# Optimization experiments

Hardware: AMD Instinct MI355X
Metric: run time of the kernel (lower is better)

The kernel has to match this reference:

```python
import jax, jax.numpy as jnp
import numpy as np

# Scalars from init_kwargs (qat_training=False inference path)
IN_ZP = 0
OUT_ZP = 0
IN_SCALE = 0.02
OUT_SCALE = 0.05
STRIDE = (1, 1)
PAD = (1, 1)      # (ph, pw); module pads (pw, pw, ph, ph) via F.pad
DIL = (1, 1)
GROUPS = 1
QMIN, QMAX = -128, 127  # get_quantized_range(8)


def setup_inputs() -> dict:
    key = jax.random.key(0)
    k1, k2, k3, k4 = jax.random.split(key, 4)
    x = jax.random.randint(k1, (32, 128, 56, 56), -128, 128, dtype=jnp.int32).astype(jnp.int8)
    weight = jax.random.randint(k2, (256, 128, 3, 3), -128, 128, dtype=jnp.int32).astype(jnp.int8)
    bias = jax.random.randint(k3, (256,), -1000, 1000, dtype=jnp.int32)
    weight_scale = jax.random.uniform(k4, (256,), minval=1e-3, maxval=1e-2, dtype=jnp.float32)
    return {"x": x, "weight": weight, "bias": bias, "weight_scale": weight_scale}


def reference(x, weight, bias, weight_scale):
    # Pad spatial dims with the input zero point (matches F.pad(..., value=input_zero_point))
    xp = jnp.pad(x.astype(jnp.int32),
                 ((0, 0), (0, 0), (PAD[0], PAD[0]), (PAD[1], PAD[1])),
                 constant_values=IN_ZP)
    # Exact int32-accumulate convolution (torch CPU path)
    acc = jax.lax.conv_general_dilated(
        xp, weight.astype(jnp.int32),
        window_strides=STRIDE, padding='VALID', rhs_dilation=DIL,
        dimension_numbers=('NCHW', 'OIHW', 'NCHW'),
        feature_group_count=GROUPS, preferred_element_type=jnp.int32)
    acc = acc + bias[None, :, None, None]
    # Per-output-channel requantization
    scale = (IN_SCALE * weight_scale / OUT_SCALE)[None, :, None, None]
    out = acc.astype(jnp.float32) * scale + OUT_ZP
    out = jnp.clip(jnp.round(out), QMIN, QMAX).astype(jnp.int8)
    return out
```

## Files before the change

### kernel.cpp

```cpp
#include <hip/hip_runtime.h>
#include <hip/hip_bf16.h>
#include <stdint.h>


#define NB   32
#define CIN  128
#define HO   56
#define WO   56
#define KOUT 256
#define HP   58
#define ROWB (HP * CIN)

typedef int v4i  __attribute__((ext_vector_type(4)));
typedef int v16i __attribute__((ext_vector_type(16)));

static __device__ __forceinline__ void gload_lds16(const int8_t* g, int8_t* l) {
  __builtin_amdgcn_global_load_lds(
      (const __attribute__((address_space(1))) void*)g,
      (__attribute__((address_space(3))) void*)l, 16, 0, 0);
}

__global__ __launch_bounds__(256) void pack_x_kernel(const int* __restrict__ x,
                                                     int8_t* __restrict__ xp) {
  __shared__ int t32[128][57];
  const int tid = threadIdx.x;
  const int r = blockIdx.x;
  const int n = blockIdx.y;
  const bool interior = (r >= 1) && (r <= HO);

  if (interior) {
    const int h = r - 1;
    const int* xrow = x + ((size_t)(n * CIN) * HO + h) * WO;
    #pragma unroll
    for (int it = 0; it < 7; ++it) {
      const int j = it * 256 + tid;
      const int c = j / 14;
      const int w4 = j - c * 14;
      const int4 v = *reinterpret_cast<const int4*>(xrow + c * 3136 + w4 * 4);
      t32[c][w4 * 4 + 0] = v.x;
      t32[c][w4 * 4 + 1] = v.y;
      t32[c][w4 * 4 + 2] = v.z;
      t32[c][w4 * 4 + 3] = v.w;
    }
  }
  __syncthreads();
  #pragma unroll
  for (int it = 0; it < 8; ++it) {
    const int i = it * 256 + tid;
    if (i < HP * 32) {
      const int w = i >> 5;
      const int c4 = i & 31;
      int vv = 0;
      if (interior && w >= 1 && w <= WO) {
        const int b0 = t32[c4 * 4 + 0][w - 1] & 0xff;
        const int b1 = t32[c4 * 4 + 1][w - 1] & 0xff;
        const int b2 = t32[c4 * 4 + 2][w - 1] & 0xff;
        const int b3 = t32[c4 * 4 + 3][w - 1];
        vv = b0 | (b1 << 8) | (b2 << 16) | (b3 << 24);
      }
      *reinterpret_cast<int*>(xp + ((size_t)(n * HP + r) * HP + w) * CIN + c4 * 4) = vv;
    }
  }
}

__global__ __launch_bounds__(256) void pack_w_kernel(const int* __restrict__ wgt,
                                                     int8_t* __restrict__ wq) {
  const int wid = blockIdx.x * 256 + threadIdx.x;
  const int wi = wid & 3;
  const int ci = wid >> 2;
  const int kt = ci / 4608;
  const int r  = ci - kt * 4608;
  const int tap = r >> 9;
  const int r2  = r & 511;
  const int cc  = r2 >> 6;
  const int ch  = r2 & 63;
  const int k_global = kt * 64 + ch;
  const int cin0 = cc * 16 + wi * 4;
  const int base = (k_global * CIN + cin0) * 9 + tap;
  const int v0 = wgt[base];
  const int v1 = wgt[base + 9];
  const int v2 = wgt[base + 18];
  const int v3 = wgt[base + 27];
  reinterpret_cast<int*>(wq)[wid] =
      (v0 & 0xff) | ((v1 & 0xff) << 8) | ((v2 & 0xff) << 16) | (v3 << 24);
}

__global__ __launch_bounds__(512, 2) void conv_kernel(const int8_t* __restrict__ xp,
                                                      const int8_t* __restrict__ wq,
                                                      const int* __restrict__ bias,
                                                      const float* __restrict__ wscale,
                                                      int* __restrict__ out) {
  __shared__ __align__(16) int8_t lw[9 * 8 * 64 * 16];
  __shared__ __align__(16) int8_t lx[10 * HP * 8 * 16];
  __shared__ int   bsh[64];
  __shared__ float ssh[64];

  const int tid = threadIdx.x;
  const int kt = blockIdx.x;
  const int h0 = blockIdx.y * 8;
  const int n_img = blockIdx.z;

  const int lane = tid & 63;
  const int wr = tid >> 6;
  const int p0 = lane & 31;
  const int half = lane >> 5;

  const int8_t* xg = xp + ((size_t)(n_img * HP) + h0) * ROWB;
  const int8_t* wqt = wq + (size_t)kt * 73728;

  #pragma unroll
  for (int it = 0; it < 9; ++it) {
    const int j = it * 512 + tid;
    gload_lds16(wqt + j * 16, lw + j * 16);
  }
  #pragma unroll
  for (int it = 0; it < 10; ++it) {
    const int i = it * 512 + tid;
    if (i < 10 * HP * 8) {
      const int pf = i >> 3;
      const int cc = (i & 7) ^ (pf & 7);
      gload_lds16(xg + pf * CIN + (cc << 4), lx + i * 16);
    }
  }
  if (tid < 64) {
    const int ch = kt * 64 + tid;
    bsh[tid] = bias[ch];
    ssh[tid] = (0.02f * wscale[ch]) / 0.05f;
  }
  __syncthreads();

  v16i acc[2][2];
  #pragma unroll
  for (int mt = 0; mt < 2; ++mt)
    #pragma unroll
    for (int nt = 0; nt < 2; ++nt)
      #pragma unroll
      for (int e = 0; e < 16; ++e) acc[mt][nt][e] = 0;

  #pragma unroll
  for (int tap = 0; tap < 9; ++tap) {
    const int kh = tap / 3, kw = tap % 3;
    const int8_t* lwt = lw + tap * 8192;
    const int pfb = (wr + kh) * HP + kw;
    #pragma unroll
    for (int ks = 0; ks < 4; ++ks) {
      const int cch = 2 * ks + half;
      const v4i a0 = *reinterpret_cast<const v4i*>(lwt + cch * 1024 + p0 * 16);
      const v4i a1 = *reinterpret_cast<const v4i*>(lwt + cch * 1024 + (32 + p0) * 16);
      #pragma unroll
      for (int nt = 0; nt < 2; ++nt) {
        const int pf = pfb + nt * 32 + p0;
        const v4i b = *reinterpret_cast<const v4i*>(
            lx + pf * CIN + ((cch ^ (pf & 7)) << 4));
        acc[0][nt] = __builtin_amdgcn_mfma_i32_32x32x32_i8(a0, b, acc[0][nt], 0, 0, 0);
        acc[1][nt] = __builtin_amdgcn_mfma_i32_32x32x32_i8(a1, b, acc[1][nt], 0, 0, 0);
      }
    }
  }

  const int h = h0 + wr;
  #pragma unroll
  for (int mt = 0; mt < 2; ++mt) {
    #pragma unroll
    for (int r = 0; r < 16; ++r) {
      const int cl = mt * 32 + (r & 3) + 8 * (r >> 2) + 4 * half;
      const int bi = bsh[cl];
      const float sc = ssh[cl];
      int* ob = out + (((size_t)(n_img * KOUT + kt * 64 + cl)) * HO + h) * WO;
      #pragma unroll
      for (int nt = 0; nt < 2; ++nt) {
        const int w = nt * 32 + p0;
        if (w < WO) {
          float v = (float)(acc[mt][nt][r] + bi) * sc;
          v = rintf(v);
          v = fminf(fmaxf(v, -128.0f), 127.0f);
          ob[w] = (int)v;
        }
      }
    }
  }
}

extern "C" void kernel_launch(void* const* d_in, const int* in_sizes, int n_in,
                              void* d_out, int out_size, void* d_ws, size_t ws_size,
                              hipStream_t stream) {
  const int* x = (const int*)d_in[0];
  const int* wgt = (const int*)d_in[1];
  const int* bias = (const int*)d_in[2];
  const float* wscale = (const float*)d_in[3];
  int* out = (int*)d_out;

  int8_t* xp = (int8_t*)d_ws;
  int8_t* wq = (int8_t*)d_ws + (size_t)NB * HP * ROWB;

  pack_x_kernel<<<dim3(HP, NB), 256, 0, stream>>>(x, xp);
  pack_w_kernel<<<288, 256, 0, stream>>>(wgt, wq);
  conv_kernel<<<dim3(4, 7, 32), 512, 0, stream>>>(xp, wq, bias, wscale, out);
}
```

Measured before the change: 185.0 us.

## Retile conv to 128 channels per block with double-buffered per-tap weight prefetch

Changes the conv block tile from 64 output channels by 8 rows with 512 threads to 128 channels by 4 rows with 256 threads. Each wave now holds four M tiles, so every loaded input fragment feeds twice as many MFMAs. Weights are staged per tap into a double-buffered LDS slice and prefetched one tap ahead, which shrinks LDS footprint. In exchange it adds a barrier per tap, more accumulator registers, and more input halo loaded per output row.

```diff
diff --git a/kernel.cpp b/kernel.cpp
--- a/kernel.cpp
+++ b/kernel.cpp
@@ -68,13 +68,13 @@
   const int wid = blockIdx.x * 256 + threadIdx.x;
   const int wi = wid & 3;
   const int ci = wid >> 2;
-  const int kt = ci / 4608;
-  const int r  = ci - kt * 4608;
-  const int tap = r >> 9;
-  const int r2  = r & 511;
-  const int cc  = r2 >> 6;
-  const int ch  = r2 & 63;
-  const int k_global = kt * 64 + ch;
+  const int ktb = ci / 9216;
+  const int r  = ci - ktb * 9216;
+  const int tap = r >> 10;
+  const int r2  = r & 1023;
+  const int cc  = r2 >> 7;
+  const int ch  = r2 & 127;
+  const int k_global = ktb * 128 + ch;
   const int cin0 = cc * 16 + wi * 4;
   const int base = (k_global * CIN + cin0) * 9 + tap;
   const int v0 = wgt[base];
@@ -85,20 +85,21 @@
       (v0 & 0xff) | ((v1 & 0xff) << 8) | ((v2 & 0xff) << 16) | (v3 << 24);
 }
 
-__global__ __launch_bounds__(512, 2) void conv_kernel(const int8_t* __restrict__ xp,
+__global__ __launch_bounds__(256, 2) void conv_kernel(const int8_t* __restrict__ xp,
                                                       const int8_t* __restrict__ wq,
                                                       const int* __restrict__ bias,
                                                       const float* __restrict__ wscale,
                                                       int* __restrict__ out) {
-  __shared__ __align__(16) int8_t lw[9 * 8 * 64 * 16];
-  __shared__ __align__(16) int8_t lx[10 * HP * 8 * 16];
-  __shared__ int   bsh[64];
-  __shared__ float ssh[64];
+  __shared__ __align__(16) int8_t lw[2][8 * 128 * 16];
+  __shared__ __align__(16) int8_t lx[6 * HP * 8 * 16];
+  __shared__ int   bsh[128];
+  __shared__ float ssh[128];
 
   const int tid = threadIdx.x;
-  const int kt = blockIdx.x;
-  const int h0 = blockIdx.y * 8;
-  const int n_img = blockIdx.z;
+  const int rg = blockIdx.x;
+  const int n_img = blockIdx.y;
+  const int ktb = blockIdx.z;
+  const int h0 = rg * 4;
 
   const int lane = tid & 63;
   const int wr = tid >> 6;
@@ -106,32 +107,32 @@
   const int half = lane >> 5;
 
   const int8_t* xg = xp + ((size_t)(n_img * HP) + h0) * ROWB;
-  const int8_t* wqt = wq + (size_t)kt * 73728;
-
-  #pragma unroll
-  for (int it = 0; it < 9; ++it) {
-    const int j = it * 512 + tid;
-    gload_lds16(wqt + j * 16, lw + j * 16);
-  }
-  #pragma unroll
-  for (int it = 0; it < 10; ++it) {
-    const int i = it * 512 + tid;
-    if (i < 10 * HP * 8) {
+  const int8_t* wqt = wq + (size_t)ktb * (9 * 16384);
+
+  #pragma unroll
+  for (int it = 0; it < 11; ++it) {
+    const int i = it * 256 + tid;
+    if (i < 6 * HP * 8) {
       const int pf = i >> 3;
       const int cc = (i & 7) ^ (pf & 7);
       gload_lds16(xg + pf * CIN + (cc << 4), lx + i * 16);
     }
   }
-  if (tid < 64) {
-    const int ch = kt * 64 + tid;
+  #pragma unroll
+  for (int it = 0; it < 4; ++it) {
+    const int j = it * 256 + tid;
+    gload_lds16(wqt + j * 16, lw[0] + j * 16);
+  }
+  if (tid < 128) {
+    const int ch = ktb * 128 + tid;
     bsh[tid] = bias[ch];
     ssh[tid] = (0.02f * wscale[ch]) / 0.05f;
   }
   __syncthreads();
 
-  v16i acc[2][2];
-  #pragma unroll
-  for (int mt = 0; mt < 2; ++mt)
+  v16i acc[4][2];
+  #pragma unroll
+  for (int mt = 0; mt < 4; ++mt)
     #pragma unroll
     for (int nt = 0; nt < 2; ++nt)
       #pragma unroll
@@ -139,34 +140,47 @@
 
   #pragma unroll
   for (int tap = 0; tap < 9; ++tap) {
-    const int kh = tap / 3, kw = tap % 3;
-    const int8_t* lwt = lw + tap * 8192;
+    if (tap < 8) {
+      const int8_t* wsrc = wqt + (tap + 1) * 16384;
+      int8_t* ldst = lw[(tap + 1) & 1];
+      #pragma unroll
+      for (int it = 0; it < 4; ++it) {
+        const int j = it * 256 + tid;
+        gload_lds16(wsrc + j * 16, ldst + j * 16);
+      }
+    }
+    const int kh = tap / 3, kw = tap - kh * 3;
+    const int8_t* lwt = lw[tap & 1];
     const int pfb = (wr + kh) * HP + kw;
     #pragma unroll
     for (int ks = 0; ks < 4; ++ks) {
       const int cch = 2 * ks + half;
-      const v4i a0 = *reinterpret_cast<const v4i*>(lwt + cch * 1024 + p0 * 16);
-      const v4i a1 = *reinterpret_cast<const v4i*>(lwt + cch * 1024 + (32 + p0) * 16);
+      v4i a[4];
+      #pragma unroll
+      for (int mt = 0; mt < 4; ++mt)
+        a[mt] = *reinterpret_cast<const v4i*>(lwt + cch * 2048 + (mt * 32 + p0) * 16);
       #pragma unroll
       for (int nt = 0; nt < 2; ++nt) {
         const int pf = pfb + nt * 32 + p0;
         const v4i b = *reinterpret_cast<const v4i*>(
             lx + pf * CIN + ((cch ^ (pf & 7)) << 4));
-        acc[0][nt] = __builtin_amdgcn_mfma_i32_32x32x32_i8(a0, b, acc[0][nt], 0, 0, 0);
-        acc[1][nt] = __builtin_amdgcn_mfma_i32_32x32x32_i8(a1, b, acc[1][nt], 0, 0, 0);
-      }
-    }
+        #pragma unroll
+        for (int mt = 0; mt < 4; ++mt)
+          acc[mt][nt] = __builtin_amdgcn_mfma_i32_32x32x32_i8(a[mt], b, acc[mt][nt], 0, 0, 0);
+      }
+    }
+    __syncthreads();
   }
 
   const int h = h0 + wr;
   #pragma unroll
-  for (int mt = 0; mt < 2; ++mt) {
+  for (int mt = 0; mt < 4; ++mt) {
     #pragma unroll
     for (int r = 0; r < 16; ++r) {
       const int cl = mt * 32 + (r & 3) + 8 * (r >> 2) + 4 * half;
       const int bi = bsh[cl];
       const float sc = ssh[cl];
-      int* ob = out + (((size_t)(n_img * KOUT + kt * 64 + cl)) * HO + h) * WO;
+      int* ob = out + (((size_t)(n_img * KOUT + ktb * 128 + cl)) * HO + h) * WO;
       #pragma unroll
       for (int nt = 0; nt < 2; ++nt) {
         const int w = nt * 32 + p0;
@@ -195,5 +209,5 @@
 
   pack_x_kernel<<<dim3(HP, NB), 256, 0, stream>>>(x, xp);
   pack_w_kernel<<<288, 256, 0, stream>>>(wgt, wq);
-  conv_kernel<<<dim3(4, 7, 32), 512, 0, stream>>>(xp, wq, bias, wscale, out);
-}
+  conv_kernel<<<dim3(14, 32, 2), 256, 0, stream>>>(xp, wq, bias, wscale, out);
+}
```

Result: no change. 182.5 us (-1.4%).

## Read packed input directly from global memory and drop LDS input staging

Applied to the files above, without the earlier changes.

The packed input layout becomes channel-chunk-major per row (8 chunks of 58×16 bytes), so each lane's B operand is a contiguous 16-byte global load and the input no longer needs to be staged into LDS. Only the weights stay in LDS, which cuts LDS use and lets launch bounds rise to 4 blocks per SM. The grid is reordered so blocks sharing an image and weight tile run close together, and the tap loop is no longer unrolled. The trade-off is that the MFMA loop now waits on global or L2 latency for every input fragment, with no LDS reuse across waves.

```diff
diff --git a/kernel.cpp b/kernel.cpp
--- a/kernel.cpp
+++ b/kernel.cpp
@@ -48,8 +48,10 @@
   for (int it = 0; it < 8; ++it) {
     const int i = it * 256 + tid;
     if (i < HP * 32) {
-      const int w = i >> 5;
-      const int c4 = i & 31;
+      const int wi = i & 3;
+      const int w = (i >> 2) % HP;
+      const int cc = (i >> 2) / HP;
+      const int c4 = cc * 4 + wi;
       int vv = 0;
       if (interior && w >= 1 && w <= WO) {
         const int b0 = t32[c4 * 4 + 0][w - 1] & 0xff;
@@ -58,7 +60,8 @@
         const int b3 = t32[c4 * 4 + 3][w - 1];
         vv = b0 | (b1 << 8) | (b2 << 16) | (b3 << 24);
       }
-      *reinterpret_cast<int*>(xp + ((size_t)(n * HP + r) * HP + w) * CIN + c4 * 4) = vv;
+      *reinterpret_cast<int*>(
+          xp + ((size_t)(n * HP + r) * 8 + cc) * 928 + w * 16 + wi * 4) = vv;
     }
   }
 }
@@ -85,42 +88,31 @@
       (v0 & 0xff) | ((v1 & 0xff) << 8) | ((v2 & 0xff) << 16) | (v3 << 24);
 }
 
-__global__ __launch_bounds__(512, 2) void conv_kernel(const int8_t* __restrict__ xp,
+__global__ __launch_bounds__(512, 4) void conv_kernel(const int8_t* __restrict__ xp,
                                                       const int8_t* __restrict__ wq,
                                                       const int* __restrict__ bias,
                                                       const float* __restrict__ wscale,
                                                       int* __restrict__ out) {
   __shared__ __align__(16) int8_t lw[9 * 8 * 64 * 16];
-  __shared__ __align__(16) int8_t lx[10 * HP * 8 * 16];
   __shared__ int   bsh[64];
   __shared__ float ssh[64];
 
   const int tid = threadIdx.x;
-  const int kt = blockIdx.x;
-  const int h0 = blockIdx.y * 8;
-  const int n_img = blockIdx.z;
+  const int rg = blockIdx.x;
+  const int n_img = blockIdx.y;
+  const int kt = blockIdx.z;
+  const int h0 = rg * 8;
 
   const int lane = tid & 63;
   const int wr = tid >> 6;
   const int p0 = lane & 31;
   const int half = lane >> 5;
 
-  const int8_t* xg = xp + ((size_t)(n_img * HP) + h0) * ROWB;
   const int8_t* wqt = wq + (size_t)kt * 73728;
-
   #pragma unroll
   for (int it = 0; it < 9; ++it) {
     const int j = it * 512 + tid;
     gload_lds16(wqt + j * 16, lw + j * 16);
-  }
-  #pragma unroll
-  for (int it = 0; it < 10; ++it) {
-    const int i = it * 512 + tid;
-    if (i < 10 * HP * 8) {
-      const int pf = i >> 3;
-      const int cc = (i & 7) ^ (pf & 7);
-      gload_lds16(xg + pf * CIN + (cc << 4), lx + i * 16);
-    }
   }
   if (tid < 64) {
     const int ch = kt * 64 + tid;
@@ -137,24 +129,25 @@
       #pragma unroll
       for (int e = 0; e < 16; ++e) acc[mt][nt][e] = 0;
 
-  #pragma unroll
+  const int8_t* xb = xp + ((size_t)(n_img * HP + h0 + wr) * 8) * 928 + p0 * 16;
+
+  #pragma unroll 1
   for (int tap = 0; tap < 9; ++tap) {
-    const int kh = tap / 3, kw = tap % 3;
+    const int kh = (tap >= 3) + (tap >= 6);
+    const int kw = tap - 3 * kh;
     const int8_t* lwt = lw + tap * 8192;
-    const int pfb = (wr + kh) * HP + kw;
+    const int8_t* xrow = xb + (kh * 8) * 928 + kw * 16;
     #pragma unroll
     for (int ks = 0; ks < 4; ++ks) {
       const int cch = 2 * ks + half;
       const v4i a0 = *reinterpret_cast<const v4i*>(lwt + cch * 1024 + p0 * 16);
-      const v4i a1 = *reinterpret_cast<const v4i*>(lwt + cch * 1024 + (32 + p0) * 16);
-      #pragma unroll
-      for (int nt = 0; nt < 2; ++nt) {
-        const int pf = pfb + nt * 32 + p0;
-        const v4i b = *reinterpret_cast<const v4i*>(
-            lx + pf * CIN + ((cch ^ (pf & 7)) << 4));
-        acc[0][nt] = __builtin_amdgcn_mfma_i32_32x32x32_i8(a0, b, acc[0][nt], 0, 0, 0);
-        acc[1][nt] = __builtin_amdgcn_mfma_i32_32x32x32_i8(a1, b, acc[1][nt], 0, 0, 0);
-      }
+      const v4i a1 = *reinterpret_cast<const v4i*>(lwt + cch * 1024 + p0 * 16 + 512);
+      const v4i b0 = *reinterpret_cast<const v4i*>(xrow + cch * 928);
+      const v4i b1 = *reinterpret_cast<const v4i*>(xrow + cch * 928 + 512);
+      acc[0][0] = __builtin_amdgcn_mfma_i32_32x32x32_i8(a0, b0, acc[0][0], 0, 0, 0);
+      acc[1][0] = __builtin_amdgcn_mfma_i32_32x32x32_i8(a1, b0, acc[1][0], 0, 0, 0);
+      acc[0][1] = __builtin_amdgcn_mfma_i32_32x32x32_i8(a0, b1, acc[0][1], 0, 0, 0);
+      acc[1][1] = __builtin_amdgcn_mfma_i32_32x32x32_i8(a1, b1, acc[1][1], 0, 0, 0);
     }
   }
 
@@ -195,5 +188,5 @@
 
   pack_x_kernel<<<dim3(HP, NB), 256, 0, stream>>>(x, xp);
   pack_w_kernel<<<288, 256, 0, stream>>>(wgt, wq);
-  conv_kernel<<<dim3(4, 7, 32), 512, 0, stream>>>(xp, wq, bias, wscale, out);
+  conv_kernel<<<dim3(7, 32, 4), 512, 0, stream>>>(xp, wq, bias, wscale, out);
 }
```

New measurement: 189.2 us. 2.3% more time.
